# Kernel tuning notes

Hardware: AMD Instinct MI355X
Metric: run time of the kernel (lower is better)

The kernel has to match this reference:

```python
import jax, jax.numpy as jnp
import numpy as np

IN_NEURONS = 32
OUT_NEURONS = 32
MODES_SPACE = 16
MODES_TIME = 32
SCALE = 1.0 / (IN_NEURONS * OUT_NEURONS)


def setup_inputs() -> dict:
    key = jax.random.key(0)
    k1, k2, k3 = jax.random.split(key, 3)
    B, T, X, Y = 2, 64, 128, 128
    x = jax.random.normal(k1, (B, IN_NEURONS, T, X, Y), dtype=jnp.float32)
    wshape = (IN_NEURONS, OUT_NEURONS, MODES_TIME, 2 * MODES_SPACE, 2 * MODES_SPACE)
    # torch.rand(dtype=cfloat): real and imag parts uniform in [0,1), then scaled
    w_real = SCALE * jax.random.uniform(k2, wshape, dtype=jnp.float32)
    w_imag = SCALE * jax.random.uniform(k3, wshape, dtype=jnp.float32)
    return {"x": x, "w_real": w_real, "w_imag": w_imag}


def reference(x, w_real, w_imag):
    weights = (w_real + 1j * w_imag).astype(jnp.complex64)  # [i, o, t, 2m, 2m]
    B = x.shape[0]
    T, X, Y = x.shape[-3], x.shape[-2], x.shape[-1]
    m = MODES_SPACE

    x_ft = jnp.fft.rfftn(x, axes=(-3, -2, -1))            # [B, I, T, X, Y//2+1]
    x_ft = jnp.fft.fftshift(x_ft, axes=(-2, -1))
    midX, midY = x_ft.shape[-2] // 2, x_ft.shape[-1] // 2

    # central spectral block, low time modes: [B, I, MODES_TIME, 2m, 2m]
    block = x_ft[..., :MODES_TIME, midX - m:midX + m, midY - m:midY + m]
    # faithful to source einsum: contracts input time-mode dim ('i') against
    # weights' in dim, input channel dim ('o') broadcast-matched to out dim
    out_block = jnp.einsum('boixy,iotxy->botxy', block, weights)

    out_ft = jnp.zeros((B, OUT_NEURONS, MODES_TIME, x_ft.shape[-2], x_ft.shape[-1]),
                       dtype=jnp.complex64)
    out_ft = out_ft.at[..., midX - m:midX + m, midY - m:midY + m].set(out_block)
    out_ft = jnp.fft.fftshift(out_ft, axes=(-2, -1))
    # irfftn pads the (short) time-frequency axis with zeros up to T
    out = jnp.fft.irfftn(out_ft, s=(T, X, Y), axes=(-3, -2, -1))
    return out.astype(jnp.float32)
```

## Files before the change

### kernel.cpp

```cpp
#include <hip/hip_runtime.h>


#define PI_F 3.14159265358979323846f

static constexpr size_t OFF_TWFX  = 0;
static constexpr size_t OFF_TWFY  = 32768;
static constexpr size_t OFF_TWFT  = 65536;
static constexpr size_t OFF_TWIT  = 81920;
static constexpr size_t OFF_TWIX  = 98304;
static constexpr size_t OFF_TWIYR = 131072;
static constexpr size_t OFF_TWIYI = 147456;
static constexpr size_t OFF_A     = 163840;
static constexpr size_t OFF_C     = OFF_A;
static constexpr size_t OFF_D     = OFF_A + 16777216ULL;
static constexpr size_t OFF_B     = OFF_A + 134217728ULL;

__device__ __forceinline__ void cmadd(float2& a, float2 u, float2 v) {
  a.x = fmaf(u.x, v.x, fmaf(-u.y, v.y, a.x));
  a.y = fmaf(u.x, v.y, fmaf( u.y, v.x, a.y));
}

__global__ void init_tables(char* __restrict__ ws) {
  int idx = blockIdx.x * 256 + threadIdx.x;
  if (idx >= 20480) return;
  float2* twFX  = (float2*)(ws + OFF_TWFX);
  float2* twFY  = (float2*)(ws + OFF_TWFY);
  float2* twFT  = (float2*)(ws + OFF_TWFT);
  float2* twIT  = (float2*)(ws + OFF_TWIT);
  float2* twIX  = (float2*)(ws + OFF_TWIX);
  float*  twIYr = (float*)(ws + OFF_TWIYR);
  float*  twIYi = (float*)(ws + OFF_TWIYI);

  if (idx < 4096) {
    int x = idx >> 5, l = idx & 31;
    int r = (((l - 16) * x) % 128 + 128) % 128;
    float a = -2.0f * PI_F * (float)r / 128.0f;
    float s, c; sincosf(a, &s, &c);
    twFX[idx] = make_float2(c, s);
  } else if (idx < 8192) {
    int k = idx - 4096;
    int y = k >> 5, j = k & 31;
    int f = (j >= 16) ? (j - 16) : (j + 49);
    int r = (f * y) % 128;
    float a = -2.0f * PI_F * (float)r / 128.0f;
    float s, c; sincosf(a, &s, &c);
    twFY[k] = make_float2(c, s);
  } else if (idx < 10240) {
    int k = idx - 8192;
    int tau = k >> 5, i = k & 31;
    int r = (i * tau) % 64;
    float a = -2.0f * PI_F * (float)r / 64.0f;
    float s, c; sincosf(a, &s, &c);
    twFT[k] = make_float2(c, s);
  } else if (idx < 12288) {
    int k = idx - 10240;
    int tau = k >> 5, t = k & 31;
    int r = (t * tau) % 64;
    float a = 2.0f * PI_F * (float)r / 64.0f;
    float s, c; sincosf(a, &s, &c);
    const float n = 1.0f / 1048576.0f;
    twIT[k] = make_float2(c * n, s * n);
  } else if (idx < 16384) {
    int k = idx - 12288;
    int Xp = k >> 5, l = k & 31;
    int r = (((l - 16) * Xp) % 128 + 128) % 128;
    float a = 2.0f * PI_F * (float)r / 128.0f;
    float s, c; sincosf(a, &s, &c);
    twIX[k] = make_float2(c, s);
  } else {
    int k = idx - 16384;
    int j = k >> 7, Yp = k & 127;
    int g = (j + 48) % 65;
    int r = (g * Yp) % 128;
    float a = 2.0f * PI_F * (float)r / 128.0f;
    float s, c; sincosf(a, &s, &c);
    bool edge = (j == 16) || (j == 17);
    float sc = edge ? 1.0f : 2.0f;
    twIYr[k] = sc * c;
    twIYi[k] = edge ? 0.0f : (-sc * s);
  }
}

__global__ void __launch_bounds__(256) k_fwd_x(const float* __restrict__ x,
                                               float2* __restrict__ S1,
                                               const float2* __restrict__ twFX) {
  __shared__ float2 tw[2048];
  for (int i = threadIdx.x; i < 2048; i += 256) tw[i] = twFX[i];
  __syncthreads();
  int slab = blockIdx.x * 2 + (threadIdx.x >> 7);
  int y = threadIdx.x & 127;
  const float* xp = x + (size_t)slab * 16384;
  float2 acc[32];
#pragma unroll
  for (int l = 0; l < 32; ++l) acc[l] = make_float2(0.f, 0.f);
  for (int xx = 0; xx < 64; ++xx) {
    float v0 = xp[xx * 128 + y];
    float v1 = xp[(xx + 64) * 128 + y];
    float ue = v0 + v1;
    float uo = v0 - v1;
    const float2* twr = &tw[xx * 32];
#pragma unroll
    for (int l = 0; l < 32; ++l) {
      float u = (l & 1) ? uo : ue;
      acc[l].x = fmaf(u, twr[l].x, acc[l].x);
      acc[l].y = fmaf(u, twr[l].y, acc[l].y);
    }
  }
  float2* outp = S1 + (size_t)slab * 4096;
#pragma unroll
  for (int l = 0; l < 32; ++l) outp[l * 128 + y] = acc[l];
}

__global__ void __launch_bounds__(256) k_fwd_y(const float2* __restrict__ S1,
                                               float2* __restrict__ S2,
                                               const float2* __restrict__ twFY) {
  __shared__ float2 tw[2048];
  __shared__ float2 rows[2048];
  for (int i = threadIdx.x; i < 2048; i += 256) tw[i] = twFY[i];
  const float2* src = S1 + (size_t)blockIdx.x * 2048;
  for (int i = threadIdx.x; i < 2048; i += 256) rows[i] = src[i];
  __syncthreads();
  int j = threadIdx.x & 31;
  int rslot = threadIdx.x >> 5;
  bool fodd = (j < 16) ? ((j & 1) == 0) : ((j & 1) == 1);
  float sgn = fodd ? -1.0f : 1.0f;
  float2 acc[2];
  acc[0] = make_float2(0.f, 0.f);
  acc[1] = make_float2(0.f, 0.f);
  for (int y = 0; y < 64; ++y) {
    float2 t = tw[y * 32 + j];
#pragma unroll
    for (int k = 0; k < 2; ++k) {
      float2 a = rows[(rslot * 2 + k) * 128 + y];
      float2 b = rows[(rslot * 2 + k) * 128 + y + 64];
      float2 u = make_float2(fmaf(sgn, b.x, a.x), fmaf(sgn, b.y, a.y));
      cmadd(acc[k], u, t);
    }
  }
  float2* dst = S2 + (size_t)blockIdx.x * 16 * 32;
#pragma unroll
  for (int k = 0; k < 2; ++k) dst[(rslot * 2 + k) * 32 + j] = acc[k];
}

__global__ void __launch_bounds__(256) k_fwd_t(const float2* __restrict__ S2,
                                               float2* __restrict__ S3,
                                               const float2* __restrict__ twFT) {
  __shared__ float2 tw[1024];
  for (int i = threadIdx.x; i < 1024; i += 256) tw[i] = twFT[i];
  __syncthreads();
  int bc = blockIdx.x >> 3;
  int sg = (blockIdx.x >> 1) & 3;
  int ih = blockIdx.x & 1;
  int s = sg * 256 + threadIdx.x;
  const float2* in = S2 + (size_t)bc * 65536 + s;
  float2 acc[16];
#pragma unroll
  for (int q = 0; q < 16; ++q) acc[q] = make_float2(0.f, 0.f);
  for (int tau = 0; tau < 32; ++tau) {
    float2 v0 = in[(size_t)tau * 1024];
    float2 v1 = in[(size_t)(tau + 32) * 1024];
    float2 ue = make_float2(v0.x + v1.x, v0.y + v1.y);
    float2 uo = make_float2(v0.x - v1.x, v0.y - v1.y);
    const float2* twr = &tw[tau * 32 + ih * 16];
#pragma unroll
    for (int q = 0; q < 16; ++q) cmadd(acc[q], (q & 1) ? uo : ue, twr[q]);
  }
  float2* outp = S3 + (size_t)bc * 32768 + (size_t)(ih * 16) * 1024 + s;
#pragma unroll
  for (int q = 0; q < 16; ++q) outp[(size_t)q * 1024] = acc[q];
}

__global__ void __launch_bounds__(256, 2) k_einsum(const float2* __restrict__ S3,
                                                   const float* __restrict__ wr,
                                                   const float* __restrict__ wi,
                                                   float2* __restrict__ S4) {
  int o  = blockIdx.x >> 4;
  int tc = (blockIdx.x >> 2) & 3;
  int sg = blockIdx.x & 3;
  int s = sg * 256 + threadIdx.x;
  float2 blk0[32], blk1[32];
#pragma unroll
  for (int i = 0; i < 32; ++i) {
    blk0[i] = S3[(size_t)(o * 32 + i) * 1024 + s];
    blk1[i] = S3[(size_t)((32 + o) * 32 + i) * 1024 + s];
  }
  for (int tt = 0; tt < 8; ++tt) {
    int t = tc * 8 + tt;
    float2 a0 = make_float2(0.f, 0.f), a1 = make_float2(0.f, 0.f);
#pragma unroll
    for (int i = 0; i < 32; ++i) {
      size_t widx = (size_t)((i * 32 + o) * 32 + t) * 1024 + s;
      float r = wr[widx], m = wi[widx];
      a0.x = fmaf(blk0[i].x, r, fmaf(-blk0[i].y, m, a0.x));
      a0.y = fmaf(blk0[i].x, m, fmaf( blk0[i].y, r, a0.y));
      a1.x = fmaf(blk1[i].x, r, fmaf(-blk1[i].y, m, a1.x));
      a1.y = fmaf(blk1[i].x, m, fmaf( blk1[i].y, r, a1.y));
    }
    S4[(size_t)(o * 32 + t) * 1024 + s] = a0;
    S4[(size_t)((32 + o) * 32 + t) * 1024 + s] = a1;
  }
}

__global__ void __launch_bounds__(256) k_inv_t(const float2* __restrict__ S4,
                                               float2* __restrict__ S5,
                                               const float2* __restrict__ twIT) {
  __shared__ float2 tw[1024];
  for (int i = threadIdx.x; i < 1024; i += 256) tw[i] = twIT[i];
  __syncthreads();
  int bo = blockIdx.x >> 2;
  int sg = blockIdx.x & 3;
  int s = sg * 256 + threadIdx.x;
  float2 in[32];
#pragma unroll
  for (int t = 0; t < 32; ++t) in[t] = S4[(size_t)bo * 32768 + (size_t)t * 1024 + s];
  float2* outp = S5 + (size_t)bo * 65536 + s;
  for (int tau = 0; tau < 32; ++tau) {
    float2 e = make_float2(0.f, 0.f), o = make_float2(0.f, 0.f);
    const float2* twr = &tw[tau * 32];
#pragma unroll
    for (int t = 0; t < 32; ++t) cmadd((t & 1) ? o : e, in[t], twr[t]);
    outp[(size_t)tau * 1024]        = make_float2(e.x + o.x, e.y + o.y);
    outp[(size_t)(tau + 32) * 1024] = make_float2(e.x - o.x, e.y - o.y);
  }
}

__global__ void __launch_bounds__(256) k_inv_x(const float2* __restrict__ S5,
                                               float2* __restrict__ S6,
                                               const float2* __restrict__ twIX) {
  __shared__ float2 tw[2048];
  __shared__ float4 inb4[512];
  float2* inb_s = (float2*)inb4;
  for (int i = threadIdx.x; i < 2048; i += 256) tw[i] = twIX[i];
  const float4* src4 = (const float4*)(S5 + (size_t)blockIdx.x * 1024);
  for (int i = threadIdx.x; i < 512; i += 256) inb4[i] = src4[i];
  __syncthreads();
  int j  = threadIdx.x & 31;
  int xs = threadIdx.x >> 5;
  float2 inb[32];
#pragma unroll
  for (int l = 0; l < 32; ++l) inb[l] = inb_s[l * 32 + j];
  float2* dst = S6 + (size_t)blockIdx.x * 4096;
  for (int it = 0; it < 8; ++it) {
    int Xp = xs * 8 + it;
    float2 e = make_float2(0.f, 0.f), o = make_float2(0.f, 0.f);
    const float2* twr = &tw[Xp * 32];
#pragma unroll
    for (int l = 0; l < 32; ++l) cmadd((l & 1) ? o : e, inb[l], twr[l]);
    dst[Xp * 32 + j]        = make_float2(e.x + o.x, e.y + o.y);
    dst[(Xp + 64) * 32 + j] = make_float2(e.x - o.x, e.y - o.y);
  }
}

__global__ void __launch_bounds__(256) k_inv_y(const float2* __restrict__ S6,
                                               float* __restrict__ out,
                                               const float* __restrict__ twIYr,
                                               const float* __restrict__ twIYi) {
  __shared__ float4 rows4[1024];
  float2* rows = (float2*)rows4;
  const float4* src4 = (const float4*)(S6 + (size_t)blockIdx.x * 2048);
  for (int i = threadIdx.x; i < 1024; i += 256) rows4[i] = src4[i];
  int Yp = threadIdx.x & 63;
  int rg = threadIdx.x >> 6;
  float cr[32], ci[32];
#pragma unroll
  for (int jj = 0; jj < 32; ++jj) {
    cr[jj] = twIYr[jj * 128 + Yp];
    ci[jj] = twIYi[jj * 128 + Yp];
  }
  __syncthreads();
  float* dst = out + (size_t)blockIdx.x * 8192;
  for (int rr = 0; rr < 16; ++rr) {
    int r = rg * 16 + rr;
    float e0 = 0.f, e1 = 0.f, o0 = 0.f, o1 = 0.f;
#pragma unroll
    for (int jj = 0; jj < 32; ++jj) {
      float2 v = rows[r * 32 + jj];
      const bool ge = (jj <= 16) ? ((jj & 1) == 0) : ((jj & 1) == 1);
      const int half = (jj >> 1) & 1;
      float& tgt = ge ? (half ? e1 : e0) : (half ? o1 : o0);
      tgt = fmaf(v.x, cr[jj], fmaf(v.y, ci[jj], tgt));
    }
    float E = e0 + e1, O = o0 + o1;
    dst[(size_t)r * 128 + Yp]      = E + O;
    dst[(size_t)r * 128 + Yp + 64] = E - O;
  }
}

extern "C" void kernel_launch(void* const* d_in, const int* in_sizes, int n_in,
                              void* d_out, int out_size, void* d_ws, size_t ws_size,
                              hipStream_t stream) {
  (void)in_sizes; (void)n_in; (void)out_size; (void)ws_size;
  const float* x  = (const float*)d_in[0];
  const float* wr = (const float*)d_in[1];
  const float* wi = (const float*)d_in[2];
  float* out = (float*)d_out;
  char* ws = (char*)d_ws;

  const float2* twFX  = (const float2*)(ws + OFF_TWFX);
  const float2* twFY  = (const float2*)(ws + OFF_TWFY);
  const float2* twFT  = (const float2*)(ws + OFF_TWFT);
  const float2* twIT  = (const float2*)(ws + OFF_TWIT);
  const float2* twIX  = (const float2*)(ws + OFF_TWIX);
  const float*  twIYr = (const float*)(ws + OFF_TWIYR);
  const float*  twIYi = (const float*)(ws + OFF_TWIYI);
  float2* S1 = (float2*)(ws + OFF_A);
  float2* S2 = (float2*)(ws + OFF_B);
  float2* S3 = (float2*)(ws + OFF_C);
  float2* S4 = (float2*)(ws + OFF_D);
  float2* S5 = (float2*)(ws + OFF_B);
  float2* S6 = (float2*)(ws + OFF_A);

  init_tables<<<dim3(80), dim3(256), 0, stream>>>(ws);
  k_fwd_x <<<dim3(2048), dim3(256), 0, stream>>>(x, S1, twFX);
  k_fwd_y <<<dim3(8192), dim3(256), 0, stream>>>(S1, S2, twFY);
  k_fwd_t <<<dim3(512),  dim3(256), 0, stream>>>(S2, S3, twFT);
  k_einsum<<<dim3(512),  dim3(256), 0, stream>>>(S3, wr, wi, S4);
  k_inv_t <<<dim3(256),  dim3(256), 0, stream>>>(S4, S5, twIT);
  k_inv_x <<<dim3(4096), dim3(256), 0, stream>>>(S5, S6, twIX);
  k_inv_y <<<dim3(8192), dim3(256), 0, stream>>>(S6, out, twIYr, twIYi);
}
```

Baseline: 1.031 ms.

## Fuse forward and inverse X/Y DFT stages and rebalance grids for occupancy

Merges the forward X and Y DFT kernels into one per-slab kernel that keeps the X-transform output in shared memory, and does the same for the inverse X and Y stages. This removes the S1 and S6 round trips through global memory. The time-DFT, einsum and inverse-time kernels are re-split across more blocks with fewer accumulators per thread, and the einsum register footprint is reduced to allow 4 blocks per CU. Twiddle factors are read as float4. The fused kernels use more shared memory per block, which may limit occupancy.

```diff
diff --git a/kernel.cpp b/kernel.cpp
--- a/kernel.cpp
+++ b/kernel.cpp
@@ -81,186 +81,196 @@
   }
 }
 
-__global__ void __launch_bounds__(256) k_fwd_x(const float* __restrict__ x,
-                                               float2* __restrict__ S1,
-                                               const float2* __restrict__ twFX) {
-  __shared__ float2 tw[2048];
-  for (int i = threadIdx.x; i < 2048; i += 256) tw[i] = twFX[i];
-  __syncthreads();
-  int slab = blockIdx.x * 2 + (threadIdx.x >> 7);
-  int y = threadIdx.x & 127;
+__global__ void __launch_bounds__(256) k_fwd_xy(const float* __restrict__ x,
+                                                float2* __restrict__ S2,
+                                                const float2* __restrict__ twFXg,
+                                                const float2* __restrict__ twFYg) {
+  __shared__ float4 twX4[1024];
+  __shared__ float4 twY4[1024];
+  __shared__ float2 mid[4096];
+  float2* twX = (float2*)twX4;
+  float2* twY = (float2*)twY4;
+  for (int i = threadIdx.x; i < 2048; i += 256) { twX[i] = twFXg[i]; twY[i] = twFYg[i]; }
+  __syncthreads();
+
+  int slab = blockIdx.x;
   const float* xp = x + (size_t)slab * 16384;
-  float2 acc[32];
-#pragma unroll
-  for (int l = 0; l < 32; ++l) acc[l] = make_float2(0.f, 0.f);
-  for (int xx = 0; xx < 64; ++xx) {
-    float v0 = xp[xx * 128 + y];
-    float v1 = xp[(xx + 64) * 128 + y];
-    float ue = v0 + v1;
-    float uo = v0 - v1;
-    const float2* twr = &tw[xx * 32];
-#pragma unroll
-    for (int l = 0; l < 32; ++l) {
-      float u = (l & 1) ? uo : ue;
-      acc[l].x = fmaf(u, twr[l].x, acc[l].x);
-      acc[l].y = fmaf(u, twr[l].y, acc[l].y);
-    }
-  }
-  float2* outp = S1 + (size_t)slab * 4096;
-#pragma unroll
-  for (int l = 0; l < 32; ++l) outp[l * 128 + y] = acc[l];
-}
-
-__global__ void __launch_bounds__(256) k_fwd_y(const float2* __restrict__ S1,
-                                               float2* __restrict__ S2,
-                                               const float2* __restrict__ twFY) {
-  __shared__ float2 tw[2048];
-  __shared__ float2 rows[2048];
-  for (int i = threadIdx.x; i < 2048; i += 256) tw[i] = twFY[i];
-  const float2* src = S1 + (size_t)blockIdx.x * 2048;
-  for (int i = threadIdx.x; i < 2048; i += 256) rows[i] = src[i];
-  __syncthreads();
-  int j = threadIdx.x & 31;
-  int rslot = threadIdx.x >> 5;
-  bool fodd = (j < 16) ? ((j & 1) == 0) : ((j & 1) == 1);
-  float sgn = fodd ? -1.0f : 1.0f;
-  float2 acc[2];
-  acc[0] = make_float2(0.f, 0.f);
-  acc[1] = make_float2(0.f, 0.f);
-  for (int y = 0; y < 64; ++y) {
-    float2 t = tw[y * 32 + j];
-#pragma unroll
-    for (int k = 0; k < 2; ++k) {
-      float2 a = rows[(rslot * 2 + k) * 128 + y];
-      float2 b = rows[(rslot * 2 + k) * 128 + y + 64];
-      float2 u = make_float2(fmaf(sgn, b.x, a.x), fmaf(sgn, b.y, a.y));
-      cmadd(acc[k], u, t);
-    }
-  }
-  float2* dst = S2 + (size_t)blockIdx.x * 16 * 32;
-#pragma unroll
-  for (int k = 0; k < 2; ++k) dst[(rslot * 2 + k) * 32 + j] = acc[k];
+
+  {
+    int y  = threadIdx.x & 127;
+    int lh = threadIdx.x >> 7;
+    float2 acc[16];
+#pragma unroll
+    for (int q = 0; q < 16; ++q) acc[q] = make_float2(0.f, 0.f);
+    for (int xx = 0; xx < 64; ++xx) {
+      float v0 = xp[xx * 128 + y];
+      float v1 = xp[(xx + 64) * 128 + y];
+      float ue = v0 + v1;
+      float uo = v0 - v1;
+      const float4* twr4 = (const float4*)&twX[xx * 32 + lh * 16];
+#pragma unroll
+      for (int p = 0; p < 8; ++p) {
+        float4 q4 = twr4[p];
+        acc[2 * p].x     = fmaf(ue, q4.x, acc[2 * p].x);
+        acc[2 * p].y     = fmaf(ue, q4.y, acc[2 * p].y);
+        acc[2 * p + 1].x = fmaf(uo, q4.z, acc[2 * p + 1].x);
+        acc[2 * p + 1].y = fmaf(uo, q4.w, acc[2 * p + 1].y);
+      }
+    }
+#pragma unroll
+    for (int q = 0; q < 16; ++q) mid[(lh * 16 + q) * 128 + y] = acc[q];
+  }
+  __syncthreads();
+
+  {
+    int j  = threadIdx.x & 31;
+    int lg = threadIdx.x >> 5;
+    bool fodd = (j < 16) ? ((j & 1) == 0) : ((j & 1) == 1);
+    float sgn = fodd ? -1.0f : 1.0f;
+    float2 acc2[4];
+#pragma unroll
+    for (int k = 0; k < 4; ++k) acc2[k] = make_float2(0.f, 0.f);
+    for (int y = 0; y < 64; ++y) {
+      float2 t = twY[y * 32 + j];
+#pragma unroll
+      for (int k = 0; k < 4; ++k) {
+        float2 a = mid[(lg * 4 + k) * 128 + y];
+        float2 b = mid[(lg * 4 + k) * 128 + y + 64];
+        float2 u = make_float2(fmaf(sgn, b.x, a.x), fmaf(sgn, b.y, a.y));
+        cmadd(acc2[k], u, t);
+      }
+    }
+    float2* dst = S2 + (size_t)slab * 1024;
+#pragma unroll
+    for (int k = 0; k < 4; ++k) dst[(lg * 4 + k) * 32 + j] = acc2[k];
+  }
 }
 
 __global__ void __launch_bounds__(256) k_fwd_t(const float2* __restrict__ S2,
                                                float2* __restrict__ S3,
                                                const float2* __restrict__ twFT) {
-  __shared__ float2 tw[1024];
+  __shared__ float4 tw4[512];
+  float2* tw = (float2*)tw4;
   for (int i = threadIdx.x; i < 1024; i += 256) tw[i] = twFT[i];
   __syncthreads();
-  int bc = blockIdx.x >> 3;
-  int sg = (blockIdx.x >> 1) & 3;
+  int bc = blockIdx.x >> 4;
+  int sg = (blockIdx.x >> 1) & 7;
   int ih = blockIdx.x & 1;
-  int s = sg * 256 + threadIdx.x;
+  int s  = sg * 128 + (threadIdx.x & 127);
+  int ibase = ih * 16 + (threadIdx.x >> 7) * 8;
   const float2* in = S2 + (size_t)bc * 65536 + s;
-  float2 acc[16];
-#pragma unroll
-  for (int q = 0; q < 16; ++q) acc[q] = make_float2(0.f, 0.f);
+  float2 acc[8];
+#pragma unroll
+  for (int q = 0; q < 8; ++q) acc[q] = make_float2(0.f, 0.f);
   for (int tau = 0; tau < 32; ++tau) {
     float2 v0 = in[(size_t)tau * 1024];
     float2 v1 = in[(size_t)(tau + 32) * 1024];
     float2 ue = make_float2(v0.x + v1.x, v0.y + v1.y);
     float2 uo = make_float2(v0.x - v1.x, v0.y - v1.y);
-    const float2* twr = &tw[tau * 32 + ih * 16];
-#pragma unroll
-    for (int q = 0; q < 16; ++q) cmadd(acc[q], (q & 1) ? uo : ue, twr[q]);
-  }
-  float2* outp = S3 + (size_t)bc * 32768 + (size_t)(ih * 16) * 1024 + s;
-#pragma unroll
-  for (int q = 0; q < 16; ++q) outp[(size_t)q * 1024] = acc[q];
-}
-
-__global__ void __launch_bounds__(256, 2) k_einsum(const float2* __restrict__ S3,
+    const float4* twr4 = (const float4*)&tw[tau * 32 + ibase];
+#pragma unroll
+    for (int p = 0; p < 4; ++p) {
+      float4 q4 = twr4[p];
+      cmadd(acc[2 * p],     ue, make_float2(q4.x, q4.y));
+      cmadd(acc[2 * p + 1], uo, make_float2(q4.z, q4.w));
+    }
+  }
+  float2* outp = S3 + (size_t)bc * 32768 + (size_t)ibase * 1024 + s;
+#pragma unroll
+  for (int q = 0; q < 8; ++q) outp[(size_t)q * 1024] = acc[q];
+}
+
+__global__ void __launch_bounds__(256, 4) k_einsum(const float2* __restrict__ S3,
                                                    const float* __restrict__ wr,
                                                    const float* __restrict__ wi,
                                                    float2* __restrict__ S4) {
-  int o  = blockIdx.x >> 4;
-  int tc = (blockIdx.x >> 2) & 3;
+  int o  = blockIdx.x >> 5;
+  int tc = (blockIdx.x >> 2) & 7;
   int sg = blockIdx.x & 3;
   int s = sg * 256 + threadIdx.x;
-  float2 blk0[32], blk1[32];
-#pragma unroll
-  for (int i = 0; i < 32; ++i) {
-    blk0[i] = S3[(size_t)(o * 32 + i) * 1024 + s];
-    blk1[i] = S3[(size_t)((32 + o) * 32 + i) * 1024 + s];
-  }
-  for (int tt = 0; tt < 8; ++tt) {
-    int t = tc * 8 + tt;
-    float2 a0 = make_float2(0.f, 0.f), a1 = make_float2(0.f, 0.f);
-#pragma unroll
-    for (int i = 0; i < 32; ++i) {
-      size_t widx = (size_t)((i * 32 + o) * 32 + t) * 1024 + s;
-      float r = wr[widx], m = wi[widx];
-      a0.x = fmaf(blk0[i].x, r, fmaf(-blk0[i].y, m, a0.x));
-      a0.y = fmaf(blk0[i].x, m, fmaf( blk0[i].y, r, a0.y));
-      a1.x = fmaf(blk1[i].x, r, fmaf(-blk1[i].y, m, a1.x));
-      a1.y = fmaf(blk1[i].x, m, fmaf( blk1[i].y, r, a1.y));
-    }
-    S4[(size_t)(o * 32 + t) * 1024 + s] = a0;
-    S4[(size_t)((32 + o) * 32 + t) * 1024 + s] = a1;
+  float2 acc0[4], acc1[4];
+#pragma unroll
+  for (int tt = 0; tt < 4; ++tt) { acc0[tt] = make_float2(0.f, 0.f); acc1[tt] = make_float2(0.f, 0.f); }
+#pragma unroll 1
+  for (int ic = 0; ic < 2; ++ic) {
+    float2 blk0[16], blk1[16];
+#pragma unroll
+    for (int q = 0; q < 16; ++q) {
+      int i = ic * 16 + q;
+      blk0[q] = S3[(size_t)(o * 32 + i) * 1024 + s];
+      blk1[q] = S3[(size_t)((32 + o) * 32 + i) * 1024 + s];
+    }
+#pragma unroll
+    for (int q = 0; q < 16; ++q) {
+      int i = ic * 16 + q;
+      size_t base = (size_t)((i * 32 + o) * 32 + tc * 4) * 1024 + s;
+      float2 b0 = blk0[q], b1 = blk1[q];
+#pragma unroll
+      for (int tt = 0; tt < 4; ++tt) {
+        float r = wr[base + (size_t)tt * 1024];
+        float m = wi[base + (size_t)tt * 1024];
+        acc0[tt].x = fmaf(b0.x, r, fmaf(-b0.y, m, acc0[tt].x));
+        acc0[tt].y = fmaf(b0.x, m, fmaf( b0.y, r, acc0[tt].y));
+        acc1[tt].x = fmaf(b1.x, r, fmaf(-b1.y, m, acc1[tt].x));
+        acc1[tt].y = fmaf(b1.x, m, fmaf( b1.y, r, acc1[tt].y));
+      }
+    }
+  }
+#pragma unroll
+  for (int tt = 0; tt < 4; ++tt) {
+    int t = tc * 4 + tt;
+    S4[(size_t)(o * 32 + t) * 1024 + s] = acc0[tt];
+    S4[(size_t)((32 + o) * 32 + t) * 1024 + s] = acc1[tt];
   }
 }
 
 __global__ void __launch_bounds__(256) k_inv_t(const float2* __restrict__ S4,
                                                float2* __restrict__ S5,
                                                const float2* __restrict__ twIT) {
-  __shared__ float2 tw[1024];
+  __shared__ float4 tw4[512];
+  float2* tw = (float2*)tw4;
   for (int i = threadIdx.x; i < 1024; i += 256) tw[i] = twIT[i];
   __syncthreads();
-  int bo = blockIdx.x >> 2;
-  int sg = blockIdx.x & 3;
-  int s = sg * 256 + threadIdx.x;
+  int bo = blockIdx.x >> 4;
+  int sg = blockIdx.x & 15;
+  int s  = sg * 64 + (threadIdx.x & 63);
+  int tq = threadIdx.x >> 6;
   float2 in[32];
 #pragma unroll
   for (int t = 0; t < 32; ++t) in[t] = S4[(size_t)bo * 32768 + (size_t)t * 1024 + s];
   float2* outp = S5 + (size_t)bo * 65536 + s;
-  for (int tau = 0; tau < 32; ++tau) {
+  for (int tt = 0; tt < 8; ++tt) {
+    int tau = tq * 8 + tt;
     float2 e = make_float2(0.f, 0.f), o = make_float2(0.f, 0.f);
-    const float2* twr = &tw[tau * 32];
-#pragma unroll
-    for (int t = 0; t < 32; ++t) cmadd((t & 1) ? o : e, in[t], twr[t]);
+    const float4* twr4 = (const float4*)&tw[tau * 32];
+#pragma unroll
+    for (int p = 0; p < 16; ++p) {
+      float4 q4 = twr4[p];
+      cmadd(e, in[2 * p],     make_float2(q4.x, q4.y));
+      cmadd(o, in[2 * p + 1], make_float2(q4.z, q4.w));
+    }
     outp[(size_t)tau * 1024]        = make_float2(e.x + o.x, e.y + o.y);
     outp[(size_t)(tau + 32) * 1024] = make_float2(e.x - o.x, e.y - o.y);
   }
 }
 
-__global__ void __launch_bounds__(256) k_inv_x(const float2* __restrict__ S5,
-                                               float2* __restrict__ S6,
-                                               const float2* __restrict__ twIX) {
-  __shared__ float2 tw[2048];
+__global__ void __launch_bounds__(256) k_inv_xy(const float2* __restrict__ S5,
+                                                float* __restrict__ out,
+                                                const float2* __restrict__ twIXg,
+                                                const float* __restrict__ twIYr,
+                                                const float* __restrict__ twIYi) {
+  __shared__ float4 twX4[1024];
   __shared__ float4 inb4[512];
+  __shared__ float4 mid4[2048];
+  float2* twX  = (float2*)twX4;
   float2* inb_s = (float2*)inb4;
-  for (int i = threadIdx.x; i < 2048; i += 256) tw[i] = twIX[i];
-  const float4* src4 = (const float4*)(S5 + (size_t)blockIdx.x * 1024);
+  float2* mid  = (float2*)mid4;
+  for (int i = threadIdx.x; i < 2048; i += 256) twX[i] = twIXg[i];
+  int slab = blockIdx.x;
+  const float4* src4 = (const float4*)(S5 + (size_t)slab * 1024);
   for (int i = threadIdx.x; i < 512; i += 256) inb4[i] = src4[i];
-  __syncthreads();
-  int j  = threadIdx.x & 31;
-  int xs = threadIdx.x >> 5;
-  float2 inb[32];
-#pragma unroll
-  for (int l = 0; l < 32; ++l) inb[l] = inb_s[l * 32 + j];
-  float2* dst = S6 + (size_t)blockIdx.x * 4096;
-  for (int it = 0; it < 8; ++it) {
-    int Xp = xs * 8 + it;
-    float2 e = make_float2(0.f, 0.f), o = make_float2(0.f, 0.f);
-    const float2* twr = &tw[Xp * 32];
-#pragma unroll
-    for (int l = 0; l < 32; ++l) cmadd((l & 1) ? o : e, inb[l], twr[l]);
-    dst[Xp * 32 + j]        = make_float2(e.x + o.x, e.y + o.y);
-    dst[(Xp + 64) * 32 + j] = make_float2(e.x - o.x, e.y - o.y);
-  }
-}
-
-__global__ void __launch_bounds__(256) k_inv_y(const float2* __restrict__ S6,
-                                               float* __restrict__ out,
-                                               const float* __restrict__ twIYr,
-                                               const float* __restrict__ twIYi) {
-  __shared__ float4 rows4[1024];
-  float2* rows = (float2*)rows4;
-  const float4* src4 = (const float4*)(S6 + (size_t)blockIdx.x * 2048);
-  for (int i = threadIdx.x; i < 1024; i += 256) rows4[i] = src4[i];
+
   int Yp = threadIdx.x & 63;
-  int rg = threadIdx.x >> 6;
   float cr[32], ci[32];
 #pragma unroll
   for (int jj = 0; jj < 32; ++jj) {
@@ -268,21 +278,58 @@
     ci[jj] = twIYi[jj * 128 + Yp];
   }
   __syncthreads();
-  float* dst = out + (size_t)blockIdx.x * 8192;
-  for (int rr = 0; rr < 16; ++rr) {
-    int r = rg * 16 + rr;
-    float e0 = 0.f, e1 = 0.f, o0 = 0.f, o1 = 0.f;
-#pragma unroll
-    for (int jj = 0; jj < 32; ++jj) {
-      float2 v = rows[r * 32 + jj];
-      const bool ge = (jj <= 16) ? ((jj & 1) == 0) : ((jj & 1) == 1);
-      const int half = (jj >> 1) & 1;
-      float& tgt = ge ? (half ? e1 : e0) : (half ? o1 : o0);
-      tgt = fmaf(v.x, cr[jj], fmaf(v.y, ci[jj], tgt));
-    }
-    float E = e0 + e1, O = o0 + o1;
-    dst[(size_t)r * 128 + Yp]      = E + O;
-    dst[(size_t)r * 128 + Yp + 64] = E - O;
+
+  {
+    int j  = threadIdx.x & 31;
+    int xs = threadIdx.x >> 5;
+    float2 inb[32];
+#pragma unroll
+    for (int l = 0; l < 32; ++l) inb[l] = inb_s[l * 32 + j];
+    for (int it = 0; it < 8; ++it) {
+      int Xp = xs * 8 + it;
+      float2 e = make_float2(0.f, 0.f), o = make_float2(0.f, 0.f);
+      const float4* twr4 = (const float4*)&twX[Xp * 32];
+#pragma unroll
+      for (int p = 0; p < 16; ++p) {
+        float4 q4 = twr4[p];
+        cmadd(e, inb[2 * p],     make_float2(q4.x, q4.y));
+        cmadd(o, inb[2 * p + 1], make_float2(q4.z, q4.w));
+      }
+      mid[Xp * 32 + j]        = make_float2(e.x + o.x, e.y + o.y);
+      mid[(Xp + 64) * 32 + j] = make_float2(e.x - o.x, e.y - o.y);
+    }
+  }
+  __syncthreads();
+
+  {
+    int rg = threadIdx.x >> 6;
+    float* dst = out + (size_t)slab * 16384;
+    for (int rr = 0; rr < 32; ++rr) {
+      int r = rg * 32 + rr;
+      const float4* row4 = (const float4*)&mid[r * 32];
+      float e0 = 0.f, e1 = 0.f, o0 = 0.f, o1 = 0.f;
+#pragma unroll
+      for (int p = 0; p < 16; ++p) {
+        float4 q4 = row4[p];
+        {
+          int jj = 2 * p;
+          const bool ge = (jj <= 16) ? ((jj & 1) == 0) : ((jj & 1) == 1);
+          float c = fmaf(q4.x, cr[jj], q4.y * ci[jj]);
+          if (ge) { if ((jj >> 1) & 1) e1 += c; else e0 += c; }
+          else    { if ((jj >> 1) & 1) o1 += c; else o0 += c; }
+        }
+        {
+          int jj = 2 * p + 1;
+          const bool ge = (jj <= 16) ? ((jj & 1) == 0) : ((jj & 1) == 1);
+          float c = fmaf(q4.z, cr[jj], q4.w * ci[jj]);
+          if (ge) { if ((jj >> 1) & 1) e1 += c; else e0 += c; }
+          else    { if ((jj >> 1) & 1) o1 += c; else o0 += c; }
+        }
+      }
+      float E = e0 + e1, O = o0 + o1;
+      dst[(size_t)r * 128 + Yp]      = E + O;
+      dst[(size_t)r * 128 + Yp + 64] = E - O;
+    }
   }
 }
 
@@ -303,19 +350,15 @@
   const float2* twIX  = (const float2*)(ws + OFF_TWIX);
   const float*  twIYr = (const float*)(ws + OFF_TWIYR);
   const float*  twIYi = (const float*)(ws + OFF_TWIYI);
-  float2* S1 = (float2*)(ws + OFF_A);
   float2* S2 = (float2*)(ws + OFF_B);
   float2* S3 = (float2*)(ws + OFF_C);
   float2* S4 = (float2*)(ws + OFF_D);
   float2* S5 = (float2*)(ws + OFF_B);
-  float2* S6 = (float2*)(ws + OFF_A);
 
   init_tables<<<dim3(80), dim3(256), 0, stream>>>(ws);
-  k_fwd_x <<<dim3(2048), dim3(256), 0, stream>>>(x, S1, twFX);
-  k_fwd_y <<<dim3(8192), dim3(256), 0, stream>>>(S1, S2, twFY);
-  k_fwd_t <<<dim3(512),  dim3(256), 0, stream>>>(S2, S3, twFT);
-  k_einsum<<<dim3(512),  dim3(256), 0, stream>>>(S3, wr, wi, S4);
-  k_inv_t <<<dim3(256),  dim3(256), 0, stream>>>(S4, S5, twIT);
-  k_inv_x <<<dim3(4096), dim3(256), 0, stream>>>(S5, S6, twIX);
-  k_inv_y <<<dim3(8192), dim3(256), 0, stream>>>(S6, out, twIYr, twIYi);
-}
+  k_fwd_xy<<<dim3(4096), dim3(256), 0, stream>>>(x, S2, twFX, twFY);
+  k_fwd_t <<<dim3(1024), dim3(256), 0, stream>>>(S2, S3, twFT);
+  k_einsum<<<dim3(1024), dim3(256), 0, stream>>>(S3, wr, wi, S4);
+  k_inv_t <<<dim3(1024), dim3(256), 0, stream>>>(S4, S5, twIT);
+  k_inv_xy<<<dim3(4096), dim3(256), 0, stream>>>(S5, out, twIX, twIYr, twIYi);
+}
```

New measurement: 903.8 us. 1.14x faster.
